# Performance work log

Hardware: AMD Instinct MI355X
Metric: run time of the kernel (lower is better)

Reference implementation:

```python
import jax, jax.numpy as jnp
import numpy as np

LATENT = 256
OUT_CH = 1
K = 16
HEADS = 64


def _conv1x1(x, W, b):
    # x: [B, Cin, ...spatial], W: [Cout, Cin], b: [Cout]
    y = jnp.einsum('oc,bc...->bo...', W, x)
    return y + b.reshape((1, -1) + (1,) * (y.ndim - 2))


def _batch_gather(x, idx):
    # x: [B, C, N], idx: [B, Nq, K] -> [B, C, Nq, K]
    return jax.vmap(lambda xb, ib: xb[:, ib])(x, idx)


def setup_inputs() -> dict:
    key = jax.random.key(0)
    ks = jax.random.split(key, 16)
    B, N, NQ = 2, 10000, 10000
    inp = {
        'latents': jax.random.normal(ks[0], (B, LATENT, N), jnp.float32),
        'pts': jax.random.normal(ks[1], (B, 3, N), jnp.float32),
        'pts_query': jax.random.normal(ks[2], (B, 3, NQ), jnp.float32),
        'proj_ids': jax.random.randint(ks[3], (B, NQ, K), 0, N, jnp.int64),
    }
    def lin(k, o, i):
        s = 1.0 / np.sqrt(i)
        k1, k2 = jax.random.split(k)
        return (jax.random.uniform(k1, (o, i), jnp.float32, -s, s),
                jax.random.uniform(k2, (o,), jnp.float32, -s, s))
    inp['W1'], inp['b1'] = lin(ks[4], LATENT, LATENT + 3)
    inp['W2'], inp['b2'] = lin(ks[5], LATENT, LATENT)
    inp['W3'], inp['b3'] = lin(ks[6], LATENT, LATENT)
    inp['Wq'], inp['bq'] = lin(ks[7], HEADS, LATENT)
    inp['Wv'], inp['bv'] = lin(ks[8], LATENT, LATENT)
    inp['W8'], inp['b8'] = lin(ks[9], OUT_CH, LATENT)
    return inp


def reference(latents, pts, pts_query, proj_ids,
              W1, b1, W2, b2, W3, b3, Wq, bq, Wv, bv, W8, b8):
    # gather neighbor latents and points: [B, C, Nq, K], [B, 3, Nq, K]
    x = _batch_gather(latents, proj_ids)
    npts = _batch_gather(pts, proj_ids)
    rel = pts_query[:, :, :, None] - npts          # [B, 3, Nq, K]
    x = jnp.concatenate([x, rel], axis=1)          # [B, C+3, Nq, K]
    x = jax.nn.relu(_conv1x1(x, W1, b1))
    x = jax.nn.relu(_conv1x1(x, W2, b2))
    x = jax.nn.relu(_conv1x1(x, W3, b3))
    query = _conv1x1(x, Wq, bq)                    # [B, 64, Nq, K]
    value = _conv1x1(x, Wv, bv)                    # [B, C, Nq, K]
    attention = jax.nn.softmax(query, axis=-1).mean(axis=1)  # [B, Nq, K]
    # weighted sum over K neighbors: [B, Nq, C] -> [B, C, Nq]
    x = jnp.einsum('bnk,bcnk->bcn', attention, value)
    x = _conv1x1(x, W8, b8)                        # [B, out_ch, Nq]
    return x
```

## Files before the change

kernel.cpp:

```cpp
#include <hip/hip_runtime.h>
#include <cstdint>
#include <cstddef>


#define NLAT 256
#define KNB 16
#define QB 4
#define MROWS 64
#define ROWB 528
#define MTSTR 16896

typedef float    f32x4  __attribute__((ext_vector_type(4)));
typedef float    f32x16 __attribute__((ext_vector_type(16)));
typedef _Float16 f16x8  __attribute__((ext_vector_type(8)));
typedef _Float16 f16x4  __attribute__((ext_vector_type(4)));

struct Smem {
  unsigned char buf[MROWS * ROWB];
  float Sp[4][MROWS];
  float Sv[MROWS];
  int sidx[MROWS];
  int is64;
};

__device__ __forceinline__ void layer_mfma32(
    unsigned char* __restrict__ buf, const unsigned short* __restrict__ Wp,
    const float* __restrict__ bias, int lane, int wave, bool relu)
{
  const int lm32 = lane & 31, h = lane >> 5;
  const char* bp = (const char*)buf + lm32 * 528 + h * 16;
  const char* wbase = (const char*)Wp + (wave * 32 + lm32) * 32 + h * 16;

  f32x16 acc[2];
  acc[0] = (f32x16)(0.f);
  acc[1] = (f32x16)(0.f);

#pragma unroll
  for (int ks = 0; ks < 16; ++ks) {
    f16x8 a = *(const f16x8*)(wbase + ks * 8192);
    f16x8 b0 = *(const f16x8*)(bp + ks * 32);
    f16x8 b1 = *(const f16x8*)(bp + MTSTR + ks * 32);
    acc[0] = __builtin_amdgcn_mfma_f32_32x32x16_f16(a, b0, acc[0], 0, 0, 0);
    acc[1] = __builtin_amdgcn_mfma_f32_32x32x16_f16(a, b1, acc[1], 0, 0, 0);
  }
  __syncthreads();
#pragma unroll
  for (int q = 0; q < 4; ++q) {
    const int ch0 = wave * 32 + q * 8 + h * 4;
    const float4 bs = *(const float4*)(bias + ch0);
    const float bb[4] = {bs.x, bs.y, bs.z, bs.w};
#pragma unroll
    for (int mt = 0; mt < 2; ++mt) {
      f16x4 v;
#pragma unroll
      for (int j = 0; j < 4; ++j) {
        float x = acc[mt][q * 4 + j] + bb[j];
        if (relu) x = fmaxf(x, 0.f);
        v[j] = (_Float16)x;
      }
      *(f16x4*)((char*)buf + (mt * 32 + lm32) * 528 + ch0 * 2) = v;
    }
  }
}

extern "C" __global__ __launch_bounds__(512, 8)
void interp_mfma(const float* __restrict__ pts,
                 const float* __restrict__ ptsq,
                 const void*  __restrict__ proj,
                 const unsigned short* __restrict__ L1pre,
                 const float* __restrict__ w1rT,
                 const unsigned short* __restrict__ W2p,
                 const unsigned short* __restrict__ W3p,
                 const unsigned short* __restrict__ Wqh,
                 const float* __restrict__ b2, const float* __restrict__ b3,
                 const float* __restrict__ bq,
                 const float* __restrict__ wv8, const float* __restrict__ c0p,
                 float* __restrict__ out,
                 int N, int NQ)
{
  __shared__ Smem sm;
  const int tid = threadIdx.x;
  const int bid = blockIdx.x;
  const int lane = tid & 63, wave = tid >> 6;
  const int lm = lane & 15, lk = lane >> 4;

  if (tid == 0) {
    const int* p = (const int*)proj;
    int z = 1;
    for (int i = 0; i < 64; ++i) z &= (p[2 * i + 1] == 0);
    sm.is64 = z;
  }
  __syncthreads();
  if (tid < MROWS) {
    long long g = (long long)bid * QB + (tid >> 4);
    long long base = g * KNB + (tid & 15);
    sm.sidx[tid] = sm.is64 ? (int)((const long long*)proj)[base]
                           : ((const int*)proj)[base];
  }
  __syncthreads();

  {
    const int row = tid & 63;
    const int part = __builtin_amdgcn_readfirstlane(tid >> 6);
    const int id = sm.sidx[row];
    const long long g = (long long)bid * QB + (row >> 4);
    const int b = (int)(g / NQ);
    const int nq = (int)(g - (long long)b * NQ);
    float rel[3];
#pragma unroll
    for (int j = 0; j < 3; ++j)
      rel[j] = ptsq[((size_t)b * 3 + j) * NQ + nq]
             - pts[((size_t)b * 3 + j) * N + id];
    const _Float16* lp = (const _Float16*)L1pre + ((size_t)b * N + id) * NLAT + part * 32;
    const float* wr0 = w1rT + part * 32;
    const float* wr1 = w1rT + 256 + part * 32;
    const float* wr2 = w1rT + 512 + part * 32;
    char* dst = (char*)sm.buf + row * 528 + part * 64;
#pragma unroll
    for (int cc = 0; cc < 4; ++cc) {
      f16x8 v = *(const f16x8*)(lp + cc * 8);
      f16x8 o;
#pragma unroll
      for (int e = 0; e < 8; ++e) {
        float x = (float)v[e] + rel[0] * wr0[cc * 8 + e]
                             + rel[1] * wr1[cc * 8 + e]
                             + rel[2] * wr2[cc * 8 + e];
        o[e] = (_Float16)fmaxf(x, 0.f);
      }
      *(f16x8*)(dst + cc * 16) = o;
    }
  }
  __syncthreads();

  layer_mfma32(sm.buf, W2p, b2, lane, wave, true);
  __syncthreads();
  layer_mfma32(sm.buf, W3p, b3, lane, wave, true);
  __syncthreads();

  if (wave < 4) {
    const char* bp16 = (const char*)sm.buf + lm * 528 + lk * 16;
    f32x4 qacc[4];
#pragma unroll
    for (int mt = 0; mt < 4; ++mt) qacc[mt] = (f32x4){0.f, 0.f, 0.f, 0.f};
    {
      const char* wqb = (const char*)Wqh + (wave * 16 + lm) * 512 + lk * 16;
#pragma unroll
      for (int ks = 0; ks < 8; ++ks) {
        f16x8 a = *(const f16x8*)(wqb + ks * 64);
#pragma unroll
        for (int mt = 0; mt < 4; ++mt) {
          f16x8 bf = *(const f16x8*)(bp16 + mt * 8448 + ks * 64);
          qacc[mt] = __builtin_amdgcn_mfma_f32_16x16x32_f16(a, bf, qacc[mt], 0, 0, 0);
        }
      }
    }
    float bqv[4];
#pragma unroll
    for (int r = 0; r < 4; ++r) bqv[r] = bq[wave * 16 + lk * 4 + r];
#pragma unroll
    for (int mt = 0; mt < 4; ++mt) {
      float sw = 0.f;
#pragma unroll
      for (int r = 0; r < 4; ++r) {
        const float qv = qacc[mt][r] + bqv[r];
        float mx = qv;
#pragma unroll
        for (int msk = 1; msk < 16; msk <<= 1) mx = fmaxf(mx, __shfl_xor(mx, msk));
        const float e = __expf(qv - mx);
        float s = e;
#pragma unroll
        for (int msk = 1; msk < 16; msk <<= 1) s += __shfl_xor(s, msk);
        sw += e / s;
      }
      sw += __shfl_xor(sw, 16);
      sw += __shfl_xor(sw, 32);
      if (lk == 0) sm.Sp[wave][mt * 16 + lm] = sw;
    }
  } else {
    const int row = (wave - 4) * 16 + lm;
    const char* sp = (const char*)sm.buf + row * 528 + lk * 16;
    float sacc = 0.f;
#pragma unroll
    for (int cc = 0; cc < 8; ++cc) {
      f16x8 v = *(const f16x8*)(sp + cc * 64);
      const int k0 = cc * 32 + lk * 8;
      const float4 w0 = *(const float4*)(wv8 + k0);
      const float4 w1 = *(const float4*)(wv8 + k0 + 4);
      sacc += (float)v[0] * w0.x + (float)v[1] * w0.y
            + (float)v[2] * w0.z + (float)v[3] * w0.w;
      sacc += (float)v[4] * w1.x + (float)v[5] * w1.y
            + (float)v[6] * w1.z + (float)v[7] * w1.w;
    }
    sacc += __shfl_xor(sacc, 16);
    sacc += __shfl_xor(sacc, 32);
    if (lk == 0) sm.Sv[row] = sacc;
  }
  __syncthreads();

  if (wave < 4) {
    const int m = wave * 16 + lm;
    const float a = (sm.Sp[0][m] + sm.Sp[1][m] + sm.Sp[2][m] + sm.Sp[3][m]) * (1.f / 64.f);
    float val = a * sm.Sv[m];
#pragma unroll
    for (int msk = 1; msk < 16; msk <<= 1) val += __shfl_xor(val, msk);
    if (lane == 0) out[(long long)bid * QB + wave] = val + c0p[0];
  }
}

extern "C" __global__ __launch_bounds__(256, 4)
void l1pre_k(const float* __restrict__ latents,
             const unsigned short* __restrict__ W1p,
             const float* __restrict__ b1,
             unsigned short* __restrict__ L1pre, int N)
{
  __shared__ unsigned char buf[MROWS * ROWB];
  const int tid = threadIdx.x;
  const int b = blockIdx.y, n0 = blockIdx.x * 64;
  const int lane = tid & 63, wave = tid >> 6;
  const int lm32 = lane & 31, h = lane >> 5;

  {
    const int nl = tid & 63;
    const int n = n0 + nl;
    const bool ok = (n < N);
#pragma unroll
    for (int jj = 0; jj < 8; ++jj) {
      const int j = (tid >> 6) + jj * 4;
      f16x8 v;
#pragma unroll
      for (int e = 0; e < 8; ++e) {
        const float x = ok ? latents[((size_t)b * NLAT + j * 8 + e) * N + n] : 0.f;
        v[e] = (_Float16)x;
      }
      *(f16x8*)((char*)buf + nl * 528 + j * 16) = v;
    }
  }
  __syncthreads();

  const char* bp = (const char*)buf + lm32 * 528 + h * 16;
  const char* wbase = (const char*)W1p + (wave * 64 + lm32) * 32 + h * 16;
  f32x16 acc[2][2];
#pragma unroll
  for (int i = 0; i < 2; ++i)
#pragma unroll
    for (int j = 0; j < 2; ++j) acc[i][j] = (f32x16)(0.f);
#pragma unroll
  for (int ks = 0; ks < 16; ++ks) {
    f16x8 a[2], bb[2];
#pragma unroll
    for (int ct = 0; ct < 2; ++ct)
      a[ct] = *(const f16x8*)(wbase + ks * 8192 + ct * 1024);
#pragma unroll
    for (int mt = 0; mt < 2; ++mt)
      bb[mt] = *(const f16x8*)(bp + mt * MTSTR + ks * 32);
#pragma unroll
    for (int ct = 0; ct < 2; ++ct)
#pragma unroll
      for (int mt = 0; mt < 2; ++mt)
        acc[ct][mt] = __builtin_amdgcn_mfma_f32_32x32x16_f16(a[ct], bb[mt], acc[ct][mt], 0, 0, 0);
  }
#pragma unroll
  for (int ct = 0; ct < 2; ++ct) {
#pragma unroll
    for (int q = 0; q < 4; ++q) {
      const int ch0 = wave * 64 + ct * 32 + q * 8 + h * 4;
      const float4 bs = *(const float4*)(b1 + ch0);
      const float bb[4] = {bs.x, bs.y, bs.z, bs.w};
#pragma unroll
      for (int mt = 0; mt < 2; ++mt) {
        const int n = n0 + mt * 32 + lm32;
        if (n < N) {
          f16x4 v;
#pragma unroll
          for (int j = 0; j < 4; ++j)
            v[j] = (_Float16)(acc[ct][mt][q * 4 + j] + bb[j]);
          *(f16x4*)((char*)L1pre + (((size_t)b * N + n) * NLAT + ch0) * 2) = v;
        }
      }
    }
  }
}

extern "C" __global__ void prep_w(const float* __restrict__ W1, const float* __restrict__ W2,
                                  const float* __restrict__ W3, const float* __restrict__ Wq,
                                  const float* __restrict__ Wv, const float* __restrict__ W8,
                                  const float* __restrict__ bv, const float* __restrict__ b8,
                                  unsigned short* W1p, unsigned short* W2p,
                                  unsigned short* W3p, unsigned short* Wqh,
                                  float* w1rT, float* wv8, float* c0) {
  const int t = blockIdx.x * 256 + threadIdx.x;
  union { _Float16 h; unsigned short u; } cv;
  if (t < 65536) {
    const int ch = t >> 8, k = t & 255;
    const int dst = (k >> 4) * 4096 + ch * 16 + (k & 15);
    cv.h = (_Float16)W1[(size_t)ch * 259 + k]; W1p[dst] = cv.u;
    cv.h = (_Float16)W2[t]; W2p[dst] = cv.u;
    cv.h = (_Float16)W3[t]; W3p[dst] = cv.u;
  }
  if (t < 16384) { cv.h = (_Float16)Wq[t]; Wqh[t] = cv.u; }
  if (t < 768) {
    const int j = t >> 8, ch = t & 255;
    w1rT[t] = W1[(size_t)ch * 259 + 256 + j];
  }
  if (t < 256) {
    float s = 0.f;
    for (int o = 0; o < 256; ++o) s += Wv[(size_t)o * 256 + t] * W8[o];
    wv8[t] = s;
  }
  if (t < 64) {
    float s = 0.f;
#pragma unroll
    for (int i = 0; i < 4; ++i) s += bv[t + 64 * i] * W8[t + 64 * i];
#pragma unroll
    for (int msk = 1; msk < 64; msk <<= 1) s += __shfl_xor(s, msk);
    if (t == 0) c0[0] = s + b8[0];
  }
}

extern "C" void kernel_launch(void* const* d_in, const int* in_sizes, int n_in,
                              void* d_out, int out_size, void* d_ws, size_t ws_size,
                              hipStream_t stream) {
  (void)n_in; (void)out_size; (void)ws_size;
  const float* latents = (const float*)d_in[0];
  const float* pts     = (const float*)d_in[1];
  const float* ptsq    = (const float*)d_in[2];
  const void*  proj    = d_in[3];
  const float* W1 = (const float*)d_in[4];  const float* b1 = (const float*)d_in[5];
  const float* W2 = (const float*)d_in[6];  const float* b2 = (const float*)d_in[7];
  const float* W3 = (const float*)d_in[8];  const float* b3 = (const float*)d_in[9];
  const float* Wq = (const float*)d_in[10]; const float* bq = (const float*)d_in[11];
  const float* Wv = (const float*)d_in[12]; const float* bv = (const float*)d_in[13];
  const float* W8 = (const float*)d_in[14]; const float* b8 = (const float*)d_in[15];
  float* out = (float*)d_out;

  const int B  = 2;
  const int N  = in_sizes[1] / (3 * B);
  const int NQ = in_sizes[2] / (3 * B);

  size_t off = 0;
  auto alloc = [&](size_t bytes) -> char* {
    char* p = (char*)d_ws + off;
    off += (bytes + 255) & ~(size_t)255;
    return p;
  };
  unsigned short* W1p = (unsigned short*)alloc(65536 * 2);
  unsigned short* W2p = (unsigned short*)alloc(65536 * 2);
  unsigned short* W3p = (unsigned short*)alloc(65536 * 2);
  unsigned short* Wqh = (unsigned short*)alloc(16384 * 2);
  float* w1rT = (float*)alloc(768 * 4);
  float* wv8  = (float*)alloc(256 * 4);
  float* c0   = (float*)alloc(4);
  unsigned short* L1pre = (unsigned short*)alloc((size_t)B * N * NLAT * 2);

  hipLaunchKernelGGL(prep_w, dim3(256), dim3(256), 0, stream,
                     W1, W2, W3, Wq, Wv, W8, bv, b8, W1p, W2p, W3p, Wqh,
                     w1rT, wv8, c0);
  hipLaunchKernelGGL(l1pre_k, dim3((N + 63) / 64, B), dim3(256), 0, stream,
                     latents, W1p, b1, L1pre, N);
  const int nblocks = (B * NQ + QB - 1) / QB;
  hipLaunchKernelGGL(interp_mfma, dim3(nblocks), dim3(512), 0, stream,
                     pts, ptsq, proj, L1pre, w1rT, W2p, W3p, Wqh,
                     b2, b3, bq, wv8, c0, out, N, NQ);
}
```

Measured before the change: 191.5 us.

## Fuse value projection into layer-3 epilogue and split query MFMA over all waves

The value·W8 dot product is now computed from fp32 layer-3 outputs inside the layer-3 epilogue, with per-wave partial sums written to shared memory and reduced at the end. This removes the separate pass in which four waves re-read the fp16 activations. The query MFMA and softmax work, previously done by only four of eight waves, is now split across all eight waves, each handling half of the rows for one head group. The cost is extra shared-memory partials and a few more FMAs and shuffles in the epilogue. Using fp32 rather than fp16-rounded activations for the value sum also changes numerics slightly.

```diff
diff --git a/kernel.cpp b/kernel.cpp
--- a/kernel.cpp
+++ b/kernel.cpp
@@ -18,14 +18,15 @@
 struct Smem {
   unsigned char buf[MROWS * ROWB];
   float Sp[4][MROWS];
-  float Sv[MROWS];
+  float Sp8[8][MROWS];
   int sidx[MROWS];
   int is64;
 };
 
 __device__ __forceinline__ void layer_mfma32(
     unsigned char* __restrict__ buf, const unsigned short* __restrict__ Wp,
-    const float* __restrict__ bias, int lane, int wave, bool relu)
+    const float* __restrict__ bias, int lane, int wave,
+    const float* __restrict__ wv8s, float* __restrict__ Sp8)
 {
   const int lm32 = lane & 31, h = lane >> 5;
   const char* bp = (const char*)buf + lm32 * 528 + h * 16;
@@ -44,21 +45,35 @@
     acc[1] = __builtin_amdgcn_mfma_f32_32x32x16_f16(a, b1, acc[1], 0, 0, 0);
   }
   __syncthreads();
+  float ssum0 = 0.f, ssum1 = 0.f;
 #pragma unroll
   for (int q = 0; q < 4; ++q) {
     const int ch0 = wave * 32 + q * 8 + h * 4;
     const float4 bs = *(const float4*)(bias + ch0);
     const float bb[4] = {bs.x, bs.y, bs.z, bs.w};
+    float wv[4] = {0.f, 0.f, 0.f, 0.f};
+    if (wv8s) {
+      const float4 w4 = *(const float4*)(wv8s + ch0);
+      wv[0] = w4.x; wv[1] = w4.y; wv[2] = w4.z; wv[3] = w4.w;
+    }
 #pragma unroll
     for (int mt = 0; mt < 2; ++mt) {
       f16x4 v;
 #pragma unroll
       for (int j = 0; j < 4; ++j) {
-        float x = acc[mt][q * 4 + j] + bb[j];
-        if (relu) x = fmaxf(x, 0.f);
+        float x = fmaxf(acc[mt][q * 4 + j] + bb[j], 0.f);
+        if (wv8s) { if (mt == 0) ssum0 += wv[j] * x; else ssum1 += wv[j] * x; }
         v[j] = (_Float16)x;
       }
       *(f16x4*)((char*)buf + (mt * 32 + lm32) * 528 + ch0 * 2) = v;
+    }
+  }
+  if (wv8s) {
+    ssum0 += __shfl_xor(ssum0, 32);
+    ssum1 += __shfl_xor(ssum1, 32);
+    if (h == 0) {
+      Sp8[wave * MROWS + lm32] = ssum0;
+      Sp8[wave * MROWS + 32 + lm32] = ssum1;
     }
   }
 }
@@ -132,75 +147,60 @@
   }
   __syncthreads();
 
-  layer_mfma32(sm.buf, W2p, b2, lane, wave, true);
-  __syncthreads();
-  layer_mfma32(sm.buf, W3p, b3, lane, wave, true);
-  __syncthreads();
-
-  if (wave < 4) {
+  layer_mfma32(sm.buf, W2p, b2, lane, wave, nullptr, nullptr);
+  __syncthreads();
+  layer_mfma32(sm.buf, W3p, b3, lane, wave, wv8, &sm.Sp8[0][0]);
+  __syncthreads();
+
+  {
+    const int hg = wave >> 1, mh = wave & 1;
     const char* bp16 = (const char*)sm.buf + lm * 528 + lk * 16;
-    f32x4 qacc[4];
-#pragma unroll
-    for (int mt = 0; mt < 4; ++mt) qacc[mt] = (f32x4){0.f, 0.f, 0.f, 0.f};
-    {
-      const char* wqb = (const char*)Wqh + (wave * 16 + lm) * 512 + lk * 16;
-#pragma unroll
-      for (int ks = 0; ks < 8; ++ks) {
-        f16x8 a = *(const f16x8*)(wqb + ks * 64);
-#pragma unroll
-        for (int mt = 0; mt < 4; ++mt) {
-          f16x8 bf = *(const f16x8*)(bp16 + mt * 8448 + ks * 64);
-          qacc[mt] = __builtin_amdgcn_mfma_f32_16x16x32_f16(a, bf, qacc[mt], 0, 0, 0);
-        }
+    f32x4 qacc[2];
+    qacc[0] = (f32x4){0.f, 0.f, 0.f, 0.f};
+    qacc[1] = (f32x4){0.f, 0.f, 0.f, 0.f};
+    const char* wqb = (const char*)Wqh + (hg * 16 + lm) * 512 + lk * 16;
+#pragma unroll
+    for (int ks = 0; ks < 8; ++ks) {
+      f16x8 a = *(const f16x8*)(wqb + ks * 64);
+#pragma unroll
+      for (int s = 0; s < 2; ++s) {
+        const int mt = 2 * mh + s;
+        f16x8 bf = *(const f16x8*)(bp16 + mt * 8448 + ks * 64);
+        qacc[s] = __builtin_amdgcn_mfma_f32_16x16x32_f16(a, bf, qacc[s], 0, 0, 0);
       }
     }
     float bqv[4];
 #pragma unroll
-    for (int r = 0; r < 4; ++r) bqv[r] = bq[wave * 16 + lk * 4 + r];
-#pragma unroll
-    for (int mt = 0; mt < 4; ++mt) {
+    for (int r = 0; r < 4; ++r) bqv[r] = bq[hg * 16 + lk * 4 + r];
+#pragma unroll
+    for (int s = 0; s < 2; ++s) {
       float sw = 0.f;
 #pragma unroll
       for (int r = 0; r < 4; ++r) {
-        const float qv = qacc[mt][r] + bqv[r];
+        const float qv = qacc[s][r] + bqv[r];
         float mx = qv;
 #pragma unroll
         for (int msk = 1; msk < 16; msk <<= 1) mx = fmaxf(mx, __shfl_xor(mx, msk));
         const float e = __expf(qv - mx);
-        float s = e;
-#pragma unroll
-        for (int msk = 1; msk < 16; msk <<= 1) s += __shfl_xor(s, msk);
-        sw += e / s;
+        float ss = e;
+#pragma unroll
+        for (int msk = 1; msk < 16; msk <<= 1) ss += __shfl_xor(ss, msk);
+        sw += e / ss;
       }
       sw += __shfl_xor(sw, 16);
       sw += __shfl_xor(sw, 32);
-      if (lk == 0) sm.Sp[wave][mt * 16 + lm] = sw;
-    }
-  } else {
-    const int row = (wave - 4) * 16 + lm;
-    const char* sp = (const char*)sm.buf + row * 528 + lk * 16;
-    float sacc = 0.f;
-#pragma unroll
-    for (int cc = 0; cc < 8; ++cc) {
-      f16x8 v = *(const f16x8*)(sp + cc * 64);
-      const int k0 = cc * 32 + lk * 8;
-      const float4 w0 = *(const float4*)(wv8 + k0);
-      const float4 w1 = *(const float4*)(wv8 + k0 + 4);
-      sacc += (float)v[0] * w0.x + (float)v[1] * w0.y
-            + (float)v[2] * w0.z + (float)v[3] * w0.w;
-      sacc += (float)v[4] * w1.x + (float)v[5] * w1.y
-            + (float)v[6] * w1.z + (float)v[7] * w1.w;
-    }
-    sacc += __shfl_xor(sacc, 16);
-    sacc += __shfl_xor(sacc, 32);
-    if (lk == 0) sm.Sv[row] = sacc;
+      if (lk == 0) sm.Sp[hg][(2 * mh + s) * 16 + lm] = sw;
+    }
   }
   __syncthreads();
 
   if (wave < 4) {
     const int m = wave * 16 + lm;
     const float a = (sm.Sp[0][m] + sm.Sp[1][m] + sm.Sp[2][m] + sm.Sp[3][m]) * (1.f / 64.f);
-    float val = a * sm.Sv[m];
+    float sv = 0.f;
+#pragma unroll
+    for (int w = 0; w < 8; ++w) sv += sm.Sp8[w][m];
+    float val = a * sv;
 #pragma unroll
     for (int msk = 1; msk < 16; msk <<= 1) val += __shfl_xor(val, msk);
     if (lane == 0) out[(long long)bid * QB + wave] = val + c0p[0];
```

Result: slower. 197.7 us (+3.3%).
